# Optimization experiments

Measured on AMD Instinct MI355X. Metric: run time of the kernel, lower is better.

Reference implementation:

```python
import jax, jax.numpy as jnp
import numpy as np
from jax import lax

B = 4096
D = 128
N = 81
H = 4
HD = D // H


def _conv(x, w, b, pad):
    y = lax.conv_general_dilated(x, w, (1, 1), [(pad, pad), (pad, pad)],
                                 dimension_numbers=('NCHW', 'OIHW', 'NCHW'))
    return y + b[None, :, None, None]


def _attn_mask():
    # per-head additive structural mask: same-row, same-col, same-box, global
    idx = jnp.arange(N)
    rows, cols = idx // 9, idx % 9
    boxes = rows // 3 * 3 + cols // 3
    same = lambda v: (v[:, None] == v[None, :]).astype(jnp.float32)
    return jnp.stack([same(rows), same(cols), same(boxes),
                      jnp.ones((N, N), jnp.float32)], 0)  # [4, 81, 81]


def setup_inputs():
    key = jax.random.key(0)
    ks = jax.random.split(key, 12)
    digits = jax.random.randint(ks[0], (B, 9, 9), 0, 10)
    s = jax.nn.one_hot(digits, 10, axis=1, dtype=jnp.float32)  # [B,10,9,9]

    def w(k, shape, fan):
        return jax.random.normal(k, shape, jnp.float32) / np.sqrt(fan)

    return {
        's': s,
        'c1_w': w(ks[1], (64, 10, 1, 1), 10), 'c1_b': jnp.zeros((64,)),
        'c2_w': w(ks[2], (128, 64, 3, 3), 64 * 9), 'c2_b': jnp.zeros((128,)),
        'c3_w': w(ks[3], (128, 128, 3, 3), 128 * 9), 'c3_b': jnp.zeros((128,)),
        'emb': 0.02 * jax.random.normal(ks[4], (1, N, D), jnp.float32),
        'in_w': w(ks[5], (3 * D, D), D), 'in_b': jnp.zeros((3 * D,)),
        'out_w': w(ks[6], (D, D), D), 'out_b': jnp.zeros((D,)),
        'ln_g': jnp.ones((D,)), 'ln_b': jnp.zeros((D,)),
        'l1_w': w(ks[7], (D, D), D), 'l1_b': jnp.zeros((D,)),
        'l2_w': w(ks[8], (D, D), D), 'l2_b': jnp.zeros((D,)),
        'pos_w': w(ks[9], (1, D), D), 'pos_b': jnp.zeros((1,)),
        'num_w': w(ks[10], (10, D), D), 'num_b': jnp.zeros((10,)),
    }


def reference(s, c1_w, c1_b, c2_w, c2_b, c3_w, c3_b, emb, in_w, in_b,
              out_w, out_b, ln_g, ln_b, l1_w, l1_b, l2_w, l2_b,
              pos_w, pos_b, num_w, num_b):
    # conv stem (note: no activation after c1, matching the torch code)
    x = _conv(s, c1_w, c1_b, 0)
    x = jax.nn.silu(_conv(x, c2_w, c2_b, 1))
    x = jax.nn.silu(_conv(x, c3_w, c3_b, 1))
    x = x.reshape(B, D, N).transpose(0, 2, 1) + emb  # [B,81,128]

    # MHA with per-head additive structural mask, no residual
    qkv = x @ in_w.T + in_b
    q, k, v = jnp.split(qkv, 3, axis=-1)
    heads = lambda t: t.reshape(B, N, H, HD).transpose(0, 2, 1, 3)
    q, k, v = heads(q), heads(k), heads(v)
    scores = jnp.einsum('bhqd,bhkd->bhqk', q, k) / np.sqrt(HD) + _attn_mask()[None]
    a = jax.nn.softmax(scores, axis=-1)          # [B,4,81,81]
    asc = a.mean(axis=1)                          # averaged attn weights
    ctx = jnp.einsum('bhqk,bhkd->bhqd', a, v).transpose(0, 2, 1, 3).reshape(B, N, D)
    x = ctx @ out_w.T + out_b

    # LayerNorm
    mu = x.mean(-1, keepdims=True)
    var = ((x - mu) ** 2).mean(-1, keepdims=True)
    x = (x - mu) / jnp.sqrt(var + 1e-5) * ln_g + ln_b

    x = jax.nn.silu(x @ l1_w.T + l1_b)
    x = jax.nn.silu(x @ l2_w.T + l2_b)

    # position head with masked softmax over empty cells
    pos_logits = (x @ pos_w.T + pos_b)[..., 0]    # [B,81]
    given = (s.argmax(1) != 0).reshape(B, N)
    pos_logits = jnp.where(given, -1e9, pos_logits)
    k1, k2 = jax.random.split(jax.random.key(42))
    pos = jax.random.categorical(k1, pos_logits)  # [B] int

    # number head at sampled position, digit 0 masked out
    num_logits = x @ num_w.T + num_b              # [B,81,10]
    o = jnp.take_along_axis(num_logits, pos[:, None, None], axis=1)[:, 0, :]
    o = o.at[:, 0].set(-jnp.inf)
    num = jax.random.categorical(k2, o)
    return pos, num, asc
```

## Files before the change

### kernel.cpp

```cpp
#include <hip/hip_runtime.h>
#include <stdint.h>
#include <math.h>


#define NB 4096

typedef unsigned short u16;
typedef _Float16 f16x8 __attribute__((ext_vector_type(8)));
typedef float f32x4 __attribute__((ext_vector_type(4)));

__device__ __forceinline__ float silu_f(float v) {
  return v / (1.0f + expf(-v));
}

__device__ __forceinline__ void splitu(float v, u16& h, u16& l) {
  _Float16 hf = (_Float16)v;
  _Float16 lf = (_Float16)((v - (float)hf) * 2048.0f);
  union { _Float16 f; u16 u; } a, b;
  a.f = hf; b.f = lf;
  h = a.u; l = b.u;
}

__device__ __forceinline__ float joinu(u16 h, u16 l) {
  union { u16 u; _Float16 f; } a, b;
  a.u = h; b.u = l;
  return (float)a.f + (float)b.f * (1.f/2048.f);
}

__device__ __forceinline__ void tf_round(uint32_t& x0, uint32_t& x1, int r) {
  x0 += x1;
  x1 = (x1 << r) | (x1 >> (32 - r));
  x1 ^= x0;
}

__device__ __forceinline__ void threefry2x32(uint32_t k0, uint32_t k1,
                                             uint32_t x0, uint32_t x1,
                                             uint32_t& o0, uint32_t& o1) {
  uint32_t k2 = k0 ^ k1 ^ 0x1BD11BDAu;
  x0 += k0; x1 += k1;
  tf_round(x0,x1,13); tf_round(x0,x1,15); tf_round(x0,x1,26); tf_round(x0,x1,6);
  x0 += k1; x1 += k2 + 1u;
  tf_round(x0,x1,17); tf_round(x0,x1,29); tf_round(x0,x1,16); tf_round(x0,x1,24);
  x0 += k2; x1 += k0 + 2u;
  tf_round(x0,x1,13); tf_round(x0,x1,15); tf_round(x0,x1,26); tf_round(x0,x1,6);
  x0 += k0; x1 += k1 + 3u;
  tf_round(x0,x1,17); tf_round(x0,x1,29); tf_round(x0,x1,16); tf_round(x0,x1,24);
  x0 += k1; x1 += k2 + 4u;
  tf_round(x0,x1,13); tf_round(x0,x1,15); tf_round(x0,x1,26); tf_round(x0,x1,6);
  x0 += k2; x1 += k0 + 5u;
  o0 = x0; o1 = x1;
}

__device__ __forceinline__ void jax_split42(uint32_t& k1a, uint32_t& k1b,
                                            uint32_t& k2a, uint32_t& k2b) {
  threefry2x32(0u, 42u, 0u, 0u, k1a, k1b);
  threefry2x32(0u, 42u, 0u, 1u, k2a, k2b);
}

__device__ __forceinline__ uint32_t jax_randbits(uint32_t ka, uint32_t kb,
                                                 uint32_t i) {
  uint32_t o0, o1;
  threefry2x32(ka, kb, 0u, i, o0, o1);
  return o0 ^ o1;
}

__device__ __forceinline__ float jax_gumbel_bits(uint32_t bits) {
  float f = __uint_as_float((bits >> 9) | 0x3f800000u) - 1.0f;
  const float tiny = 1.17549435e-38f;
  float u = fmaxf(tiny, f + tiny);
  return -logf(-logf(u));
}

__global__ __launch_bounds__(256) void k_prep(
    const float* __restrict__ c1_w, const float* __restrict__ c1_b,
    const float* __restrict__ c2_w, const float* __restrict__ c3_w,
    const float* __restrict__ out_w, const float* __restrict__ l1_w,
    const float* __restrict__ l2_w,
    float* __restrict__ T2e, u16* __restrict__ WAh, u16* __restrict__ WAl,
    u16* __restrict__ WOh, u16* __restrict__ W1h, u16* __restrict__ W2h)
{
  int idx = blockIdx.x * 256 + threadIdx.x;
  if (idx < 9*11*128) {
    int oc = idx & 127;
    int t  = idx >> 7;
    int g  = t % 11;
    int d  = t / 11;
    float acc = 0.f;
    if (g < 10) {
      int di = d / 3, dj = d % 3;
      for (int ic = 0; ic < 64; ++ic) {
        float x1 = c1_w[ic*10 + g] + c1_b[ic];
        acc += c2_w[((oc*64 + ic)*3 + di)*3 + dj] * x1;
      }
    }
    T2e[idx] = acc;
  } else if (idx < 160128) {
    int j  = idx - 12672;
    int jj = j & 7;
    int t  = j >> 3;
    int ln = t & 63;
    int t2 = t >> 6;
    int ot = t2 & 7;
    int t3 = t2 >> 3;
    int kc = t3 & 3;
    int d  = t3 >> 2;
    int oc = ot*16 + (ln & 15);
    int ic = kc*32 + (ln >> 4)*8 + jj;
    float w = c3_w[(oc*128 + ic)*9 + d];
    u16 wh, wl;
    splitu(w, wh, wl);
    WAh[j] = wh; WAl[j] = wl;
  } else if (idx < 209280) {
    int j = idx - 160128;
    int mi = j >> 14;
    int jr = j & 16383;
    int jj = jr & 7;
    int t  = jr >> 3;
    int ln = t & 63;
    int t2 = t >> 6;
    int ot = t2 & 7;
    int kc = t2 >> 3;
    int oc = ot*16 + (ln & 15);
    int k  = kc*32 + (ln >> 4)*8 + jj;
    const float* W = (mi == 0) ? out_w : (mi == 1) ? l1_w : l2_w;
    u16* Dh = (mi == 0) ? WOh : (mi == 1) ? W1h : W2h;
    u16 wh, wl;
    splitu(W[oc*128 + k], wh, wl);
    Dh[jr] = wh; Dh[16384 + jr] = wl;
  }
}

__global__ __launch_bounds__(256, 2) void k_stem(
    const float* __restrict__ s, const float* __restrict__ T2e,
    const float* __restrict__ c2_b,
    const u16* __restrict__ WAh, const u16* __restrict__ WAl,
    const float* __restrict__ c3_b, const float* __restrict__ emb,
    u16* __restrict__ xh, u16* __restrict__ xl, int* __restrict__ digits)
{
  __shared__ __align__(16) u16 x2h[121*128];
  __shared__ __align__(16) u16 x2l[121*128];
  __shared__ int dg[121];
  const int b   = blockIdx.x;
  const int tid = threadIdx.x;

  for (int i = tid; i < 1936; i += 256) {
    ((uint4*)x2h)[i] = make_uint4(0u,0u,0u,0u);
    ((uint4*)x2l)[i] = make_uint4(0u,0u,0u,0u);
  }
  if (tid < 121) dg[tid] = 10;
  __syncthreads();

  if (tid < 81) {
    const float* sp = s + (size_t)b*810 + tid;
    float dv = 0.f;
    #pragma unroll
    for (int c = 1; c < 10; ++c) dv += (float)c * sp[c*81];
    int d = (int)(dv + 0.5f);
    dg[(tid/9 + 1)*11 + (tid%9 + 1)] = d;
    digits[b*81 + tid] = d;
  }
  __syncthreads();

  for (int i = tid; i < 1296; i += 256) {
    const int p  = i >> 4;
    const int k8 = i & 15;
    const int r0 = p / 9, c0 = p - r0*9;
    const float4 b0 = *(const float4*)(c2_b + k8*8);
    const float4 b1 = *(const float4*)(c2_b + k8*8 + 4);
    float a0=b0.x, a1=b0.y, a2=b0.z, a3=b0.w;
    float a4=b1.x, a5=b1.y, a6=b1.z, a7=b1.w;
    #pragma unroll
    for (int d = 0; d < 9; ++d) {
      const int g = dg[(r0 + d/3)*11 + (c0 + d%3)];
      const float* tp = T2e + (size_t)(d*11 + g)*128 + k8*8;
      const float4 t0 = *(const float4*)tp;
      const float4 t1 = *(const float4*)(tp + 4);
      a0 += t0.x; a1 += t0.y; a2 += t0.z; a3 += t0.w;
      a4 += t1.x; a5 += t1.y; a6 += t1.z; a7 += t1.w;
    }
    float v[8];
    v[0]=silu_f(a0); v[1]=silu_f(a1); v[2]=silu_f(a2); v[3]=silu_f(a3);
    v[4]=silu_f(a4); v[5]=silu_f(a5); v[6]=silu_f(a6); v[7]=silu_f(a7);
    f16x8 hv, lv;
    #pragma unroll
    for (int j = 0; j < 8; ++j) {
      _Float16 h = (_Float16)v[j];
      hv[j] = h;
      lv[j] = (_Float16)((v[j] - (float)h) * 2048.0f);
    }
    const int row = (r0 + 1)*11 + (c0 + 1);
    const uint32_t bo = (uint32_t)row*256u + ((uint32_t)(k8 ^ (row & 15)) << 4);
    *(f16x8*)((char*)x2h + bo) = hv;
    *(f16x8*)((char*)x2l + bo) = lv;
  }
  __syncthreads();

  const int ln  = tid & 63;
  const int wv  = tid >> 6;
  const int lg  = ln >> 4;
  const int lr  = ln & 15;
  const int otB = (wv & 1) * 4;
  const int ntB = (wv >> 1) * 3;

  f32x4 accH[4][3];
  f32x4 accC[4][3];
  #pragma unroll
  for (int ot = 0; ot < 4; ++ot)
    #pragma unroll
    for (int nt = 0; nt < 3; ++nt) {
      accH[ot][nt] = (f32x4){0.f,0.f,0.f,0.f};
      accC[ot][nt] = (f32x4){0.f,0.f,0.f,0.f};
    }

  int pbase[3];
  #pragma unroll
  for (int nt = 0; nt < 3; ++nt) {
    const int c = (ntB + nt)*16 + lr;
    pbase[nt] = (c < 81) ? (c/9)*11 + (c%9) : 0;
  }
  const char* x2hB = (const char*)x2h;
  const char* x2lB = (const char*)x2l;

  for (int d = 0; d < 9; ++d) {
    const int off = (d/3)*11 + (d - (d/3)*3);
    int rowv[3];
    #pragma unroll
    for (int nt = 0; nt < 3; ++nt) rowv[nt] = pbase[nt] + off;
    #pragma unroll
    for (int kc = 0; kc < 4; ++kc) {
      f16x8 Bh[3], Bl[3];
      #pragma unroll
      for (int nt = 0; nt < 3; ++nt) {
        const uint32_t o = (uint32_t)rowv[nt]*256u +
            ((uint32_t)((kc*4 + lg) ^ (rowv[nt] & 15)) << 4);
        Bh[nt] = *(const f16x8*)(x2hB + o);
        Bl[nt] = *(const f16x8*)(x2lB + o);
      }
      const int abase = (((d*4 + kc)*8 + otB)*64 + ln)*8;
      f16x8 Ah[4], Al[4];
      #pragma unroll
      for (int ot = 0; ot < 4; ++ot) {
        Ah[ot] = *(const f16x8*)(WAh + abase + ot*512);
        Al[ot] = *(const f16x8*)(WAl + abase + ot*512);
      }
      #pragma unroll
      for (int ot = 0; ot < 4; ++ot)
        #pragma unroll
        for (int nt = 0; nt < 3; ++nt) {
          accH[ot][nt] = __builtin_amdgcn_mfma_f32_16x16x32_f16(
              Ah[ot], Bh[nt], accH[ot][nt], 0, 0, 0);
          accC[ot][nt] = __builtin_amdgcn_mfma_f32_16x16x32_f16(
              Ah[ot], Bl[nt], accC[ot][nt], 0, 0, 0);
          accC[ot][nt] = __builtin_amdgcn_mfma_f32_16x16x32_f16(
              Al[ot], Bh[nt], accC[ot][nt], 0, 0, 0);
        }
    }
  }

  #pragma unroll
  for (int nt = 0; nt < 3; ++nt) {
    const int cell = (ntB + nt)*16 + lr;
    if (cell < 81) {
      const size_t xoff = ((size_t)b*81 + cell)*128;
      #pragma unroll
      for (int ot = 0; ot < 4; ++ot) {
        const int oc = (otB + ot)*16 + lg*4;
        const float4 b3 = *(const float4*)(c3_b + oc);
        const float4 e  = *(const float4*)(emb + cell*128 + oc);
        const f32x4 hh = accH[ot][nt];
        const f32x4 cc = accC[ot][nt];
        float o0 = silu_f(hh[0] + cc[0]*(1.f/2048.f) + b3.x) + e.x;
        float o1 = silu_f(hh[1] + cc[1]*(1.f/2048.f) + b3.y) + e.y;
        float o2 = silu_f(hh[2] + cc[2]*(1.f/2048.f) + b3.z) + e.z;
        float o3 = silu_f(hh[3] + cc[3]*(1.f/2048.f) + b3.w) + e.w;
        ushort4 hv, lv;
        splitu(o0, hv.x, lv.x); splitu(o1, hv.y, lv.y);
        splitu(o2, hv.z, lv.z); splitu(o3, hv.w, lv.w);
        *(ushort4*)(xh + xoff + oc) = hv;
        *(ushort4*)(xl + xoff + oc) = lv;
      }
    }
  }
}

#define ATTN_LDS_BYTES 141568

__global__ __launch_bounds__(512, 1) void k_attn(
    const u16* __restrict__ xhg, const u16* __restrict__ xlg,
    const float* __restrict__ in_w, const float* __restrict__ in_b,
    u16* __restrict__ ctxh, u16* __restrict__ ctxl, float* __restrict__ asc)
{
  extern __shared__ char smc[];
  char*  XH   = smc;
  char*  XL   = smc + 24576;
  char*  QK   = smc + 49152;
  char*  VTH  = smc + 73728;
  char*  VTL  = smc + 81920;
  float* SC   = (float*)(smc + 90112);
  char*  PH   = smc + 90112;
  char*  PL   = smc + 114688;
  float* RINV = (float*)(smc + 140800);
  uint32_t* RCB = (uint32_t*)(smc + 141184);

  const int b   = blockIdx.x;
  const int tid = threadIdx.x;
  const int ln  = tid & 63;
  const int wv  = tid >> 6;
  const int lg  = ln >> 4;
  const int lr  = ln & 15;

  if (tid < 96) {
    const int r = tid/9, c = tid - r*9;
    const int bx = (r/3)*3 + c/3;
    RCB[tid] = (uint32_t)r | ((uint32_t)c << 8) | ((uint32_t)bx << 16);
  }
  {
    const u16* gx = xhg + (size_t)b*81*128;
    const u16* gl = xlg + (size_t)b*81*128;
    for (int i = tid; i < 1296; i += 512) {
      const int n = i >> 4, k8 = i & 15;
      const uint4 hv = *(const uint4*)(gx + n*128 + k8*8);
      const uint4 lv = *(const uint4*)(gl + n*128 + k8*8);
      const uint32_t bo = (uint32_t)n*256u + ((uint32_t)(k8 ^ (n & 15)) << 4);
      *(uint4*)(XH + bo) = hv;
      *(uint4*)(XL + bo) = lv;
    }
    for (int i = tid; i < 480; i += 512) {
      char* base = (i < 240) ? XH : XL;
      const int j = (i < 240) ? i : (i - 240);
      *(uint4*)(base + 81*256 + j*16) = make_uint4(0u,0u,0u,0u);
    }
  }

  float ascR[16];
  #pragma unroll
  for (int i = 0; i < 16; ++i) ascR[i] = 0.f;

  __syncthreads();

  for (int h = 0; h < 4; ++h) {
    if (wv < 6) {
      const int part = wv >> 1;
      const int sub  = wv & 1;
      const int rowbase = part*128 + h*32 + sub*16;
      f32x4 accH[6], accC[6];
      #pragma unroll
      for (int nt = 0; nt < 6; ++nt) {
        accH[nt] = (f32x4){0.f,0.f,0.f,0.f};
        accC[nt] = (f32x4){0.f,0.f,0.f,0.f};
      }
      for (int kc = 0; kc < 4; ++kc) {
        const float* wp = in_w + (size_t)(rowbase + lr)*128 + kc*32 + lg*8;
        f16x8 Ah, Al;
        #pragma unroll
        for (int j = 0; j < 8; ++j) {
          const float w = wp[j];
          const _Float16 hf = (_Float16)w;
          Ah[j] = hf;
          Al[j] = (_Float16)((w - (float)hf) * 2048.0f);
        }
        #pragma unroll
        for (int nt = 0; nt < 6; ++nt) {
          const int row = nt*16 + lr;
          const uint32_t o = (uint32_t)row*256u +
              ((uint32_t)((kc*4 + lg) ^ (row & 15)) << 4);
          const f16x8 Bh = *(const f16x8*)(XH + o);
          const f16x8 Bl = *(const f16x8*)(XL + o);
          accH[nt] = __builtin_amdgcn_mfma_f32_16x16x32_f16(Ah, Bh, accH[nt], 0,0,0);
          accC[nt] = __builtin_amdgcn_mfma_f32_16x16x32_f16(Ah, Bl, accC[nt], 0,0,0);
          accC[nt] = __builtin_amdgcn_mfma_f32_16x16x32_f16(Al, Bh, accC[nt], 0,0,0);
        }
      }
      const float4 bia = *(const float4*)(in_b + rowbase + lg*4);
      #pragma unroll
      for (int nt = 0; nt < 6; ++nt) {
        const int cell = nt*16 + lr;
        float v0 = accH[nt][0] + accC[nt][0]*(1.f/2048.f) + bia.x;
        float v1 = accH[nt][1] + accC[nt][1]*(1.f/2048.f) + bia.y;
        float v2 = accH[nt][2] + accC[nt][2]*(1.f/2048.f) + bia.z;
        float v3 = accH[nt][3] + accC[nt][3]*(1.f/2048.f) + bia.w;
        if (part < 2) {
          ushort4 hw, lw;
          splitu(v0, hw.x, lw.x); splitu(v1, hw.y, lw.y);
          splitu(v2, hw.z, lw.z); splitu(v3, hw.w, lw.w);
          const int sflat = part*4 + sub*2 + (lg >> 1);
          const int byo   = (lg & 1)*8;
          const uint32_t adH = (uint32_t)cell*256u +
              ((uint32_t)(sflat ^ (cell & 15)) << 4) + byo;
          const uint32_t adL = (uint32_t)cell*256u +
              ((uint32_t)((8 + sflat) ^ (cell & 15)) << 4) + byo;
          *(ushort4*)(QK + adH) = hw;
          *(ushort4*)(QK + adL) = lw;
        } else {
          float vv[4] = {v0, v1, v2, v3};
          #pragma unroll
          for (int r = 0; r < 4; ++r) {
            const int hd = sub*16 + lg*4 + r;
            u16 hh, llv;
            splitu(vv[r], hh, llv);
            const uint32_t ad = (uint32_t)hd*256u +
                ((uint32_t)((cell >> 3) ^ (hd & 15)) << 4) + (cell & 7)*2;
            *(u16*)(VTH + ad) = hh;
            *(u16*)(VTL + ad) = llv;
          }
        }
      }
    }
    __syncthreads();

    {
      const uint32_t mb = (h==0) ? 0xFFu : (h==1) ? 0xFF00u
                        : (h==2) ? 0xFF0000u : 0u;
      const int t0 = (wv*36) >> 3, t1 = ((wv + 1)*36) >> 3;
      for (int t = t0; t < t1; ++t) {
        const int qt = t/6, nt = t - (t/6)*6;
        const int ra = qt*16 + lr;
        const f16x8 Qh = *(const f16x8*)(QK + (uint32_t)ra*256u +
            ((uint32_t)(lg ^ (ra & 15)) << 4));
        const f16x8 Ql = *(const f16x8*)(QK + (uint32_t)ra*256u +
            ((uint32_t)((8 + lg) ^ (ra & 15)) << 4));
        const int rb = nt*16 + lr;
        const f16x8 Kh = *(const f16x8*)(QK + (uint32_t)rb*256u +
            ((uint32_t)((4 + lg) ^ (rb & 15)) << 4));
        const f16x8 Kl = *(const f16x8*)(QK + (uint32_t)rb*256u +
            ((uint32_t)((12 + lg) ^ (rb & 15)) << 4));
        f32x4 aH = (f32x4){0.f,0.f,0.f,0.f};
        f32x4 aC = (f32x4){0.f,0.f,0.f,0.f};
        aH = __builtin_amdgcn_mfma_f32_16x16x32_f16(Qh, Kh, aH, 0,0,0);
        aC = __builtin_amdgcn_mfma_f32_16x16x32_f16(Qh, Kl, aC, 0,0,0);
        aC = __builtin_amdgcn_mfma_f32_16x16x32_f16(Ql, Kh, aC, 0,0,0);
        const int kcell = nt*16 + lr;
        const uint32_t kk = RCB[kcell];
        #pragma unroll
        for (int r = 0; r < 4; ++r) {
          const int q = qt*16 + lg*4 + r;
          const uint32_t qq = RCB[q];
          const float msk = (((qq ^ kk) & mb) == 0u) ? 1.f : 0.f;
          SC[q*132 + kcell] =
              (aH[r] + aC[r]*(1.f/2048.f)) * 0.17677669529663687f + msk;
        }
      }
    }
    __syncthreads();

    if (tid < 324) {
      const int row = tid >> 2, sub = tid & 3;
      float* sr = SC + row*132;
      const int kb = sub*24;
      const int ke = (sub == 3) ? 81 : kb + 24;
      float m = -1e30f;
      for (int k = kb; k < ke; ++k) m = fmaxf(m, sr[k]);
      m = fmaxf(m, __shfl_xor(m, 1));
      m = fmaxf(m, __shfl_xor(m, 2));
      float ss = 0.f;
      for (int k = kb; k < ke; ++k) {
        const float e = __expf(sr[k] - m);
        sr[k] = e;
        ss += e;
      }
      if (sub == 3) {
        #pragma unroll
        for (int k = 81; k < 96; ++k) sr[k] = 0.f;
      }
      ss += __shfl_xor(ss, 1);
      ss += __shfl_xor(ss, 2);
      if (sub == 0) RINV[row] = 1.0f / ss;
    }
    __syncthreads();

    float pa[2][8];
    #pragma unroll
    for (int i = 0; i < 2; ++i) {
      const int idx = tid + i*512;
      if (idx < 972) {
        const int q = idx / 12, k8 = idx - q*12;
        const float rv = RINV[q];
        const float* sp = SC + q*132 + k8*8;
        const float4 p0 = *(const float4*)sp;
        const float4 p1 = *(const float4*)(sp + 4);
        pa[i][0] = p0.x*rv; pa[i][1] = p0.y*rv;
        pa[i][2] = p0.z*rv; pa[i][3] = p0.w*rv;
        pa[i][4] = p1.x*rv; pa[i][5] = p1.y*rv;
        pa[i][6] = p1.z*rv; pa[i][7] = p1.w*rv;
        #pragma unroll
        for (int j = 0; j < 8; ++j) ascR[i*8 + j] += pa[i][j];
      }
    }
    __syncthreads();
    #pragma unroll
    for (int i = 0; i < 2; ++i) {
      const int idx = tid + i*512;
      if (idx < 972) {
        const int q = idx / 12, k8 = idx - q*12;
        union { u16 u[8]; uint4 v; } hw, lw;
        #pragma unroll
        for (int j = 0; j < 8; ++j) splitu(pa[i][j], hw.u[j], lw.u[j]);
        const uint32_t ad = (uint32_t)q*256u +
            ((uint32_t)(k8 ^ (q & 15)) << 4);
        *(uint4*)(PH + ad) = hw.v;
        *(uint4*)(PL + ad) = lw.v;
      }
    }
    __syncthreads();

    for (int t = wv; t < 12; t += 8) {
      const int ot = t/6, nt = t - (t/6)*6;
      f32x4 aH = (f32x4){0.f,0.f,0.f,0.f};
      f32x4 aC = (f32x4){0.f,0.f,0.f,0.f};
      #pragma unroll
      for (int kc = 0; kc < 3; ++kc) {
        const int ra = ot*16 + lr;
        const uint32_t oa = (uint32_t)ra*256u +
            ((uint32_t)((kc*4 + lg) ^ (ra & 15)) << 4);
        const f16x8 Vh = *(const f16x8*)(VTH + oa);
        const f16x8 Vl = *(const f16x8*)(VTL + oa);
        const int rb = nt*16 + lr;
        const uint32_t ob = (uint32_t)rb*256u +
            ((uint32_t)((kc*4 + lg) ^ (rb & 15)) << 4);
        const f16x8 Pf  = *(const f16x8*)(PH + ob);
        const f16x8 Pl2 = *(const f16x8*)(PL + ob);
        aH = __builtin_amdgcn_mfma_f32_16x16x32_f16(Vh, Pf,  aH, 0,0,0);
        aC = __builtin_amdgcn_mfma_f32_16x16x32_f16(Vh, Pl2, aC, 0,0,0);
        aC = __builtin_amdgcn_mfma_f32_16x16x32_f16(Vl, Pf,  aC, 0,0,0);
      }
      const int cell = nt*16 + lr;
      if (cell < 81) {
        const size_t co = ((size_t)b*81 + cell)*128 + h*32 + ot*16 + lg*4;
        ushort4 hw, lw;
        float r0 = aH[0] + aC[0]*(1.f/2048.f);
        float r1 = aH[1] + aC[1]*(1.f/2048.f);
        float r2 = aH[2] + aC[2]*(1.f/2048.f);
        float r3 = aH[3] + aC[3]*(1.f/2048.f);
        splitu(r0, hw.x, lw.x); splitu(r1, hw.y, lw.y);
        splitu(r2, hw.z, lw.z); splitu(r3, hw.w, lw.w);
        *(ushort4*)(ctxh + co) = hw;
        *(ushort4*)(ctxl + co) = lw;
      }
    }
    __syncthreads();
  }

  #pragma unroll
  for (int i = 0; i < 2; ++i) {
    const int idx = tid + i*512;
    if (idx < 972) {
      const int q = idx / 12, k8 = idx - q*12;
      #pragma unroll
      for (int j = 0; j < 8; ++j) {
        const int k = k8*8 + j;
        if (k < 81) asc[(size_t)b*6561 + q*81 + k] = 0.25f * ascR[i*8 + j];
      }
    }
  }
}

#define POST_LDS_BYTES 105664

__global__ __launch_bounds__(512, 1) void k_post(
    const u16* __restrict__ ctxh, const u16* __restrict__ ctxl,
    const u16* __restrict__ WOh,  const float* __restrict__ out_b,
    const float* __restrict__ ln_g, const float* __restrict__ ln_b,
    const u16* __restrict__ W1h,  const float* __restrict__ l1_b,
    const u16* __restrict__ W2h,  const float* __restrict__ l2_b,
    const float* __restrict__ pos_w, const float* __restrict__ pos_b,
    const float* __restrict__ num_w, const float* __restrict__ num_b,
    const int* __restrict__ digits,  float* __restrict__ dout)
{
  extern __shared__ char smc[];
  char*  YH   = smc;
  char*  YL   = smc + 24576;
  char*  ZH   = smc + 49152;
  char*  ZL   = smc + 73728;
  float* red1 = (float*)(smc + 98304);
  float* red2 = (float*)(smc + 101376);
  float* mu   = (float*)(smc + 104448);
  float* rstd = (float*)(smc + 104832);
  float* vals = (float*)(smc + 105216);
  int*   posi = (int*)(smc + 105600);

  const int b   = blockIdx.x;
  const int tid = threadIdx.x;
  const int ln  = tid & 63;
  const int wv  = tid >> 6;
  const int lg  = ln >> 4;
  const int lr  = ln & 15;
  const int ocb = wv*16 + lg*4;

  {
    const u16* gh = ctxh + (size_t)b*81*128;
    const u16* gl = ctxl + (size_t)b*81*128;
    for (int i = tid; i < 1296; i += 512) {
      const int n = i >> 4, k8 = i & 15;
      const uint4 hv = *(const uint4*)(gh + n*128 + k8*8);
      const uint4 lv = *(const uint4*)(gl + n*128 + k8*8);
      const uint32_t bo = (uint32_t)n*256u + ((uint32_t)(k8 ^ (n & 15)) << 4);
      *(uint4*)(YH + bo) = hv;
      *(uint4*)(YL + bo) = lv;
    }
    for (int i = tid; i < 480; i += 512) {
      char* base = (i < 240) ? YH : YL;
      const int j = (i < 240) ? i : (i - 240);
      *(uint4*)(base + 81*256 + j*16) = make_uint4(0u,0u,0u,0u);
    }
  }
  __syncthreads();

  f32x4 aH[6], aC[6];
  #define GEMM6(BH, BL, WT)                                               \
    {                                                                     \
      _Pragma("unroll")                                                   \
      for (int nt = 0; nt < 6; ++nt) {                                    \
        aH[nt] = (f32x4){0.f,0.f,0.f,0.f};                                \
        aC[nt] = (f32x4){0.f,0.f,0.f,0.f};                                \
      }                                                                   \
      for (int kc = 0; kc < 4; ++kc) {                                    \
        const int ab = ((kc*8 + wv)*64 + ln)*8;                           \
        const f16x8 Ah = *(const f16x8*)((WT) + ab);                      \
        const f16x8 Al = *(const f16x8*)((WT) + 16384 + ab);              \
        _Pragma("unroll")                                                 \
        for (int nt = 0; nt < 6; ++nt) {                                  \
          const int row = nt*16 + lr;                                     \
          const uint32_t o = (uint32_t)row*256u +                         \
              ((uint32_t)((kc*4 + lg) ^ (row & 15)) << 4);                \
          const f16x8 Bh = *(const f16x8*)((BH) + o);                     \
          const f16x8 Bl = *(const f16x8*)((BL) + o);                     \
          aH[nt] = __builtin_amdgcn_mfma_f32_16x16x32_f16(Ah, Bh, aH[nt], 0,0,0); \
          aC[nt] = __builtin_amdgcn_mfma_f32_16x16x32_f16(Ah, Bl, aC[nt], 0,0,0); \
          aC[nt] = __builtin_amdgcn_mfma_f32_16x16x32_f16(Al, Bh, aC[nt], 0,0,0); \
        }                                                                 \
      }                                                                   \
    }

  GEMM6(YH, YL, WOh);
  float y[6][4];
  {
    const float4 bv = *(const float4*)(out_b + ocb);
    #pragma unroll
    for (int nt = 0; nt < 6; ++nt) {
      y[nt][0] = aH[nt][0] + aC[nt][0]*(1.f/2048.f) + bv.x;
      y[nt][1] = aH[nt][1] + aC[nt][1]*(1.f/2048.f) + bv.y;
      y[nt][2] = aH[nt][2] + aC[nt][2]*(1.f/2048.f) + bv.z;
      y[nt][3] = aH[nt][3] + aC[nt][3]*(1.f/2048.f) + bv.w;
    }
  }

  #pragma unroll
  for (int nt = 0; nt < 6; ++nt) {
    float s1 = y[nt][0] + y[nt][1] + y[nt][2] + y[nt][3];
    s1 += __shfl_xor(s1, 16);
    s1 += __shfl_xor(s1, 32);
    if (ln < 16) red1[(nt*16 + lr)*8 + wv] = s1;
  }
  __syncthreads();
  if (tid < 96) {
    float s = 0.f;
    #pragma unroll
    for (int w = 0; w < 8; ++w) s += red1[tid*8 + w];
    mu[tid] = s * (1.0f/128.0f);
  }
  __syncthreads();
  #pragma unroll
  for (int nt = 0; nt < 6; ++nt) {
    const float m = mu[nt*16 + lr];
    float d0 = y[nt][0]-m, d1 = y[nt][1]-m, d2 = y[nt][2]-m, d3 = y[nt][3]-m;
    float s2 = d0*d0 + d1*d1 + d2*d2 + d3*d3;
    s2 += __shfl_xor(s2, 16);
    s2 += __shfl_xor(s2, 32);
    if (ln < 16) red2[(nt*16 + lr)*8 + wv] = s2;
  }
  __syncthreads();
  if (tid < 96) {
    float s = 0.f;
    #pragma unroll
    for (int w = 0; w < 8; ++w) s += red2[tid*8 + w];
    rstd[tid] = 1.0f / sqrtf(s * (1.0f/128.0f) + 1e-5f);
  }
  __syncthreads();
  {
    const float4 g  = *(const float4*)(ln_g + ocb);
    const float4 bb = *(const float4*)(ln_b + ocb);
    #pragma unroll
    for (int nt = 0; nt < 6; ++nt) {
      const int cell = nt*16 + lr;
      const float m = mu[cell], rs = rstd[cell];
      float z0 = (y[nt][0]-m)*rs*g.x + bb.x;
      float z1 = (y[nt][1]-m)*rs*g.y + bb.y;
      float z2 = (y[nt][2]-m)*rs*g.z + bb.z;
      float z3 = (y[nt][3]-m)*rs*g.w + bb.w;
      ushort4 hw, lw;
      splitu(z0, hw.x, lw.x); splitu(z1, hw.y, lw.y);
      splitu(z2, hw.z, lw.z); splitu(z3, hw.w, lw.w);
      const uint32_t ad = (uint32_t)cell*256u +
          ((uint32_t)((wv*2 + (lg >> 1)) ^ (cell & 15)) << 4) + (lg & 1)*8;
      *(ushort4*)(ZH + ad) = hw;
      *(ushort4*)(ZL + ad) = lw;
    }
  }
  __syncthreads();

  GEMM6(ZH, ZL, W1h);
  {
    const float4 bv = *(const float4*)(l1_b + ocb);
    #pragma unroll
    for (int nt = 0; nt < 6; ++nt) {
      const int cell = nt*16 + lr;
      float z0 = silu_f(aH[nt][0] + aC[nt][0]*(1.f/2048.f) + bv.x);
      float z1 = silu_f(aH[nt][1] + aC[nt][1]*(1.f/2048.f) + bv.y);
      float z2 = silu_f(aH[nt][2] + aC[nt][2]*(1.f/2048.f) + bv.z);
      float z3 = silu_f(aH[nt][3] + aC[nt][3]*(1.f/2048.f) + bv.w);
      ushort4 hw, lw;
      splitu(z0, hw.x, lw.x); splitu(z1, hw.y, lw.y);
      splitu(z2, hw.z, lw.z); splitu(z3, hw.w, lw.w);
      const uint32_t ad = (uint32_t)cell*256u +
          ((uint32_t)((wv*2 + (lg >> 1)) ^ (cell & 15)) << 4) + (lg & 1)*8;
      *(ushort4*)(YH + ad) = hw;
      *(ushort4*)(YL + ad) = lw;
    }
  }
  __syncthreads();

  GEMM6(YH, YL, W2h);
  {
    const float4 bv = *(const float4*)(l2_b + ocb);
    const float4 pw = *(const float4*)(pos_w + ocb);
    #pragma unroll
    for (int nt = 0; nt < 6; ++nt) {
      const int cell = nt*16 + lr;
      float z0 = silu_f(aH[nt][0] + aC[nt][0]*(1.f/2048.f) + bv.x);
      float z1 = silu_f(aH[nt][1] + aC[nt][1]*(1.f/2048.f) + bv.y);
      float z2 = silu_f(aH[nt][2] + aC[nt][2]*(1.f/2048.f) + bv.z);
      float z3 = silu_f(aH[nt][3] + aC[nt][3]*(1.f/2048.f) + bv.w);
      ushort4 hw, lw;
      splitu(z0, hw.x, lw.x); splitu(z1, hw.y, lw.y);
      splitu(z2, hw.z, lw.z); splitu(z3, hw.w, lw.w);
      const uint32_t ad = (uint32_t)cell*256u +
          ((uint32_t)((wv*2 + (lg >> 1)) ^ (cell & 15)) << 4) + (lg & 1)*8;
      *(ushort4*)(ZH + ad) = hw;
      *(ushort4*)(ZL + ad) = lw;
      float ps = z0*pw.x + z1*pw.y + z2*pw.z + z3*pw.w;
      ps += __shfl_xor(ps, 16);
      ps += __shfl_xor(ps, 32);
      if (ln < 16) red1[cell*8 + wv] = ps;
    }
  }
  __syncthreads();

  uint32_t k1a, k1b, k2a, k2b;
  jax_split42(k1a, k1b, k2a, k2b);

  if (tid < 81) {
    float acc = pos_b[0];
    #pragma unroll
    for (int w = 0; w < 8; ++w) acc += red1[tid*8 + w];
    if (digits[b*81 + tid] != 0) acc = -1e9f;
    uint32_t bits = jax_randbits(k1a, k1b, (uint32_t)(b*81 + tid));
    vals[tid] = acc + jax_gumbel_bits(bits);
  }
  __syncthreads();
  if (tid == 0) {
    float best = vals[0]; int bi = 0;
    for (int n = 1; n < 81; ++n)
      if (vals[n] > best) { best = vals[n]; bi = n; }
    *posi = bi;
    dout[b] = (float)bi;
  }
  __syncthreads();
  const int pos = *posi;

  if (tid < 80) {
    const int d = tid >> 3, j = tid & 7;
    float ssum = 0.f;
    #pragma unroll
    for (int c = 0; c < 16; ++c) {
      const int k = j*16 + c;
      const uint32_t ad = (uint32_t)pos*256u +
          ((uint32_t)((k >> 3) ^ (pos & 15)) << 4) + (k & 7)*2;
      const float yv = joinu(*(const u16*)(ZH + ad), *(const u16*)(ZL + ad));
      ssum += yv * num_w[d*128 + k];
    }
    red2[tid] = ssum;
  }
  __syncthreads();
  if (tid < 10) {
    float acc = num_b[tid];
    #pragma unroll
    for (int j = 0; j < 8; ++j) acc += red2[tid*8 + j];
    if (tid == 0) acc = -INFINITY;
    uint32_t bits = jax_randbits(k2a, k2b, (uint32_t)(b*10 + tid));
    vals[tid] = acc + jax_gumbel_bits(bits);
  }
  __syncthreads();
  if (tid == 0) {
    float best = vals[0]; int bi = 0;
    for (int d = 1; d < 10; ++d)
      if (vals[d] > best) { best = vals[d]; bi = d; }
    dout[NB + b] = (float)bi;
  }
}

extern "C" void kernel_launch(void* const* d_in, const int* in_sizes, int n_in,
                              void* d_out, int out_size, void* d_ws, size_t ws_size,
                              hipStream_t stream) {
  const float* s     = (const float*)d_in[0];
  const float* c1_w  = (const float*)d_in[1];
  const float* c1_b  = (const float*)d_in[2];
  const float* c2_w  = (const float*)d_in[3];
  const float* c2_b  = (const float*)d_in[4];
  const float* c3_w  = (const float*)d_in[5];
  const float* c3_b  = (const float*)d_in[6];
  const float* emb   = (const float*)d_in[7];
  const float* in_w  = (const float*)d_in[8];
  const float* in_b  = (const float*)d_in[9];
  const float* out_w = (const float*)d_in[10];
  const float* out_b = (const float*)d_in[11];
  const float* ln_g  = (const float*)d_in[12];
  const float* ln_b  = (const float*)d_in[13];
  const float* l1_w  = (const float*)d_in[14];
  const float* l1_b  = (const float*)d_in[15];
  const float* l2_w  = (const float*)d_in[16];
  const float* l2_b  = (const float*)d_in[17];
  const float* pos_w = (const float*)d_in[18];
  const float* pos_b = (const float*)d_in[19];
  const float* num_w = (const float*)d_in[20];
  const float* num_b = (const float*)d_in[21];

  float* ws     = (float*)d_ws;
  float* T2e    = ws;
  u16*   WAh    = (u16*)(ws + 12672);
  u16*   WAl    = (u16*)(ws + 86400);
  u16*   WOh    = (u16*)(ws + 160128);
  u16*   W1h    = (u16*)(ws + 176512);
  u16*   W2h    = (u16*)(ws + 192896);
  int*   digits = (int*)(ws + 209280);
  u16*   xh     = (u16*)(ws + 541056);
  u16*   xl     = (u16*)(ws + 21774720);
  u16*   ctxh   = (u16*)(ws + 43008384);
  u16*   ctxl   = (u16*)(ws + 43008384 + 21233664);

  float* dout = (float*)d_out;
  float* asc  = dout + 2*NB;

  hipFuncSetAttribute((const void*)k_attn,
                      hipFuncAttributeMaxDynamicSharedMemorySize,
                      ATTN_LDS_BYTES);
  hipFuncSetAttribute((const void*)k_post,
                      hipFuncAttributeMaxDynamicSharedMemorySize,
                      POST_LDS_BYTES);

  k_prep<<<dim3(818), dim3(256), 0, stream>>>(
      c1_w, c1_b, c2_w, c3_w, out_w, l1_w, l2_w,
      T2e, WAh, WAl, WOh, W1h, W2h);
  k_stem<<<dim3(NB), dim3(256), 0, stream>>>(
      s, T2e, c2_b, WAh, WAl, c3_b, emb, xh, xl, digits);
  k_attn<<<dim3(NB), dim3(512), ATTN_LDS_BYTES, stream>>>(
      xh, xl, in_w, in_b, ctxh, ctxl, asc);
  k_post<<<dim3(NB), dim3(512), POST_LDS_BYTES, stream>>>(
      ctxh, ctxl, WOh, out_b, ln_g, ln_b, W1h, l1_b, W2h, l2_b,
      pos_w, pos_b, num_w, num_b, digits, dout);
}
```

Baseline: 1.440 ms.

## Presplit QKV weights in prep, spread QKV tiles over all waves, keep softmax in registers

The in_proj weights are now split into fp16 hi/lo once in k_prep, stored in MFMA fragment order, and loaded directly as vectors instead of being converted from fp32 per block and head. The QKV projection is split into 36 tile units spread across all 8 waves instead of 6, and each wave reuses B fragments cached in registers. Softmax keeps the row values in registers and fuses normalization, asc accumulation and the P store into one pass. This removes the RINV buffer and one barrier per head. Register pressure rises (e[24], ascR[24], B fragment arrays), which could limit scheduling.

```diff
diff --git a/kernel.cpp b/kernel.cpp
--- a/kernel.cpp
+++ b/kernel.cpp
@@ -74,9 +74,11 @@
 __global__ __launch_bounds__(256) void k_prep(
     const float* __restrict__ c1_w, const float* __restrict__ c1_b,
     const float* __restrict__ c2_w, const float* __restrict__ c3_w,
+    const float* __restrict__ in_w,
     const float* __restrict__ out_w, const float* __restrict__ l1_w,
     const float* __restrict__ l2_w,
     float* __restrict__ T2e, u16* __restrict__ WAh, u16* __restrict__ WAl,
+    u16* __restrict__ WIh, u16* __restrict__ WIl,
     u16* __restrict__ WOh, u16* __restrict__ W1h, u16* __restrict__ W2h)
 {
   int idx = blockIdx.x * 256 + threadIdx.x;
@@ -127,6 +129,22 @@
     u16 wh, wl;
     splitu(W[oc*128 + k], wh, wl);
     Dh[jr] = wh; Dh[16384 + jr] = wl;
+  } else if (idx < 258432) {
+    int j  = idx - 209280;
+    int jj = j & 7;
+    int t  = j >> 3;
+    int ln = t & 63;
+    int t2 = t >> 6;
+    int kc = t2 & 3;
+    int t3 = t2 >> 2;
+    int h  = t3 / 6;
+    int pu = t3 - h*6;
+    int part = pu >> 1, sub = pu & 1;
+    int row = part*128 + h*32 + sub*16 + (ln & 15);
+    int k   = kc*32 + (ln >> 4)*8 + jj;
+    u16 wh, wl;
+    splitu(in_w[row*128 + k], wh, wl);
+    WIh[j] = wh; WIl[j] = wl;
   }
 }
 
@@ -287,7 +305,8 @@
 
 __global__ __launch_bounds__(512, 1) void k_attn(
     const u16* __restrict__ xhg, const u16* __restrict__ xlg,
-    const float* __restrict__ in_w, const float* __restrict__ in_b,
+    const u16* __restrict__ WIh, const u16* __restrict__ WIl,
+    const float* __restrict__ in_b,
     u16* __restrict__ ctxh, u16* __restrict__ ctxl, float* __restrict__ asc)
 {
   extern __shared__ char smc[];
@@ -299,7 +318,6 @@
   float* SC   = (float*)(smc + 90112);
   char*  PH   = smc + 90112;
   char*  PL   = smc + 114688;
-  float* RINV = (float*)(smc + 140800);
   uint32_t* RCB = (uint32_t*)(smc + 141184);
 
   const int b   = blockIdx.x;
@@ -332,53 +350,53 @@
     }
   }
 
-  float ascR[16];
+  const int srow = tid >> 2;
+  const int ssub = tid & 3;
+  const int skn  = (ssub == 3) ? 9 : 24;
+  float ascR[24];
   #pragma unroll
-  for (int i = 0; i < 16; ++i) ascR[i] = 0.f;
+  for (int i = 0; i < 24; ++i) ascR[i] = 0.f;
 
   __syncthreads();
 
   for (int h = 0; h < 4; ++h) {
-    if (wv < 6) {
-      const int part = wv >> 1;
-      const int sub  = wv & 1;
-      const int rowbase = part*128 + h*32 + sub*16;
-      f32x4 accH[6], accC[6];
-      #pragma unroll
-      for (int nt = 0; nt < 6; ++nt) {
-        accH[nt] = (f32x4){0.f,0.f,0.f,0.f};
-        accC[nt] = (f32x4){0.f,0.f,0.f,0.f};
-      }
-      for (int kc = 0; kc < 4; ++kc) {
-        const float* wp = in_w + (size_t)(rowbase + lr)*128 + kc*32 + lg*8;
-        f16x8 Ah, Al;
+    {
+      const int t0 = (wv*36) >> 3, t1 = ((wv + 1)*36) >> 3;
+      int curNt = -1;
+      f16x8 Bh[4], Bl[4];
+      for (int u = t0; u < t1; ++u) {
+        const int nt = u/6, pu = u - (u/6)*6;
+        if (nt != curNt) {
+          curNt = nt;
+          const int row = nt*16 + lr;
+          #pragma unroll
+          for (int kc = 0; kc < 4; ++kc) {
+            const uint32_t o = (uint32_t)row*256u +
+                ((uint32_t)((kc*4 + lg) ^ (row & 15)) << 4);
+            Bh[kc] = *(const f16x8*)(XH + o);
+            Bl[kc] = *(const f16x8*)(XL + o);
+          }
+        }
+        const int part = pu >> 1, sub = pu & 1;
+        const int rowbase = part*128 + h*32 + sub*16;
+        const u16* wph = WIh + (size_t)((h*6 + pu)*4)*512 + ln*8;
+        const u16* wpl = WIl + (size_t)((h*6 + pu)*4)*512 + ln*8;
+        f32x4 aH = (f32x4){0.f,0.f,0.f,0.f};
+        f32x4 aC = (f32x4){0.f,0.f,0.f,0.f};
         #pragma unroll
-        for (int j = 0; j < 8; ++j) {
-          const float w = wp[j];
-          const _Float16 hf = (_Float16)w;
-          Ah[j] = hf;
-          Al[j] = (_Float16)((w - (float)hf) * 2048.0f);
+        for (int kc = 0; kc < 4; ++kc) {
+          const f16x8 Ah = *(const f16x8*)(wph + kc*512);
+          const f16x8 Al = *(const f16x8*)(wpl + kc*512);
+          aH = __builtin_amdgcn_mfma_f32_16x16x32_f16(Ah, Bh[kc], aH, 0,0,0);
+          aC = __builtin_amdgcn_mfma_f32_16x16x32_f16(Ah, Bl[kc], aC, 0,0,0);
+          aC = __builtin_amdgcn_mfma_f32_16x16x32_f16(Al, Bh[kc], aC, 0,0,0);
         }
-        #pragma unroll
-        for (int nt = 0; nt < 6; ++nt) {
-          const int row = nt*16 + lr;
-          const uint32_t o = (uint32_t)row*256u +
-              ((uint32_t)((kc*4 + lg) ^ (row & 15)) << 4);
-          const f16x8 Bh = *(const f16x8*)(XH + o);
-          const f16x8 Bl = *(const f16x8*)(XL + o);
-          accH[nt] = __builtin_amdgcn_mfma_f32_16x16x32_f16(Ah, Bh, accH[nt], 0,0,0);
-          accC[nt] = __builtin_amdgcn_mfma_f32_16x16x32_f16(Ah, Bl, accC[nt], 0,0,0);
-          accC[nt] = __builtin_amdgcn_mfma_f32_16x16x32_f16(Al, Bh, accC[nt], 0,0,0);
-        }
-      }
-      const float4 bia = *(const float4*)(in_b + rowbase + lg*4);
-      #pragma unroll
-      for (int nt = 0; nt < 6; ++nt) {
+        const float4 bia = *(const float4*)(in_b + rowbase + lg*4);
+        const float v0 = aH[0] + aC[0]*(1.f/2048.f) + bia.x;
+        const float v1 = aH[1] + aC[1]*(1.f/2048.f) + bia.y;
+        const float v2 = aH[2] + aC[2]*(1.f/2048.f) + bia.z;
+        const float v3 = aH[3] + aC[3]*(1.f/2048.f) + bia.w;
         const int cell = nt*16 + lr;
-        float v0 = accH[nt][0] + accC[nt][0]*(1.f/2048.f) + bia.x;
-        float v1 = accH[nt][1] + accC[nt][1]*(1.f/2048.f) + bia.y;
-        float v2 = accH[nt][2] + accC[nt][2]*(1.f/2048.f) + bia.z;
-        float v3 = accH[nt][3] + accC[nt][3]*(1.f/2048.f) + bia.w;
         if (part < 2) {
           ushort4 hw, lw;
           splitu(v0, hw.x, lw.x); splitu(v1, hw.y, lw.y);
@@ -392,7 +410,7 @@
           *(ushort4*)(QK + adH) = hw;
           *(ushort4*)(QK + adL) = lw;
         } else {
-          float vv[4] = {v0, v1, v2, v3};
+          const float vv[4] = {v0, v1, v2, v3};
           #pragma unroll
           for (int r = 0; r < 4; ++r) {
             const int hd = sub*16 + lg*4 + r;
@@ -443,60 +461,46 @@
     }
     __syncthreads();
 
+    float e[24];
+    float rinv = 0.f;
     if (tid < 324) {
-      const int row = tid >> 2, sub = tid & 3;
-      float* sr = SC + row*132;
-      const int kb = sub*24;
-      const int ke = (sub == 3) ? 81 : kb + 24;
+      const float* sr = SC + srow*132 + ssub*24;
+      #pragma unroll
+      for (int q4 = 0; q4 < 6; ++q4) {
+        const float4 v = *(const float4*)(sr + q4*4);
+        e[q4*4+0] = v.x; e[q4*4+1] = v.y; e[q4*4+2] = v.z; e[q4*4+3] = v.w;
+      }
       float m = -1e30f;
-      for (int k = kb; k < ke; ++k) m = fmaxf(m, sr[k]);
+      #pragma unroll
+      for (int c = 0; c < 24; ++c)
+        if (c < skn) m = fmaxf(m, e[c]);
       m = fmaxf(m, __shfl_xor(m, 1));
       m = fmaxf(m, __shfl_xor(m, 2));
       float ss = 0.f;
-      for (int k = kb; k < ke; ++k) {
-        const float e = __expf(sr[k] - m);
-        sr[k] = e;
-        ss += e;
-      }
-      if (sub == 3) {
-        #pragma unroll
-        for (int k = 81; k < 96; ++k) sr[k] = 0.f;
+      #pragma unroll
+      for (int c = 0; c < 24; ++c) {
+        const float ex = (c < skn) ? __expf(e[c] - m) : 0.f;
+        e[c] = ex;
+        ss += ex;
       }
       ss += __shfl_xor(ss, 1);
       ss += __shfl_xor(ss, 2);
-      if (sub == 0) RINV[row] = 1.0f / ss;
+      rinv = 1.0f / ss;
     }
     __syncthreads();
-
-    float pa[2][8];
-    #pragma unroll
-    for (int i = 0; i < 2; ++i) {
-      const int idx = tid + i*512;
-      if (idx < 972) {
-        const int q = idx / 12, k8 = idx - q*12;
-        const float rv = RINV[q];
-        const float* sp = SC + q*132 + k8*8;
-        const float4 p0 = *(const float4*)sp;
-        const float4 p1 = *(const float4*)(sp + 4);
-        pa[i][0] = p0.x*rv; pa[i][1] = p0.y*rv;
-        pa[i][2] = p0.z*rv; pa[i][3] = p0.w*rv;
-        pa[i][4] = p1.x*rv; pa[i][5] = p1.y*rv;
-        pa[i][6] = p1.z*rv; pa[i][7] = p1.w*rv;
-        #pragma unroll
-        for (int j = 0; j < 8; ++j) ascR[i*8 + j] += pa[i][j];
-      }
-    }
-    __syncthreads();
-    #pragma unroll
-    for (int i = 0; i < 2; ++i) {
-      const int idx = tid + i*512;
-      if (idx < 972) {
-        const int q = idx / 12, k8 = idx - q*12;
+    if (tid < 324) {
+      #pragma unroll
+      for (int cc = 0; cc < 3; ++cc) {
+        const int c8 = ssub*3 + cc;
         union { u16 u[8]; uint4 v; } hw, lw;
         #pragma unroll
-        for (int j = 0; j < 8; ++j) splitu(pa[i][j], hw.u[j], lw.u[j]);
-        const uint32_t ad = (uint32_t)q*256u +
-            ((uint32_t)(k8 ^ (q & 15)) << 4);
+        for (int j = 0; j < 8; ++j) {
+          const float p = e[cc*8 + j] * rinv;
+          ascR[cc*8 + j] += p;
+          splitu(p, hw.u[j], lw.u[j]);
+        }
+        const uint32_t ad = (uint32_t)srow*256u +
+            ((uint32_t)(c8 ^ (srow & 15)) << 4);
         *(uint4*)(PH + ad) = hw.v;
         *(uint4*)(PL + ad) = lw.v;
       }
@@ -540,17 +544,11 @@
     __syncthreads();
   }
 
-  #pragma unroll
-  for (int i = 0; i < 2; ++i) {
-    const int idx = tid + i*512;
-    if (idx < 972) {
-      const int q = idx / 12, k8 = idx - q*12;
-      #pragma unroll
-      for (int j = 0; j < 8; ++j) {
-        const int k = k8*8 + j;
-        if (k < 81) asc[(size_t)b*6561 + q*81 + k] = 0.25f * ascR[i*8 + j];
-      }
-    }
+  if (tid < 324) {
+    float* ap = asc + (size_t)b*6561 + srow*81 + ssub*24;
+    #pragma unroll
+    for (int c = 0; c < 24; ++c)
+      if (c < skn) ap[c] = 0.25f * ascR[c];
   }
 }
 
@@ -831,7 +829,9 @@
   u16*   WOh    = (u16*)(ws + 160128);
   u16*   W1h    = (u16*)(ws + 176512);
   u16*   W2h    = (u16*)(ws + 192896);
-  int*   digits = (int*)(ws + 209280);
+  u16*   WIh    = (u16*)(ws + 209280);
+  u16*   WIl    = (u16*)(ws + 233856);
+  int*   digits = (int*)(ws + 258432);
   u16*   xh     = (u16*)(ws + 541056);
   u16*   xl     = (u16*)(ws + 21774720);
   u16*   ctxh   = (u16*)(ws + 43008384);
@@ -847,13 +847,13 @@
                       hipFuncAttributeMaxDynamicSharedMemorySize,
                       POST_LDS_BYTES);
 
-  k_prep<<<dim3(818), dim3(256), 0, stream>>>(
-      c1_w, c1_b, c2_w, c3_w, out_w, l1_w, l2_w,
-      T2e, WAh, WAl, WOh, W1h, W2h);
+  k_prep<<<dim3(1010), dim3(256), 0, stream>>>(
+      c1_w, c1_b, c2_w, c3_w, in_w, out_w, l1_w, l2_w,
+      T2e, WAh, WAl, WIh, WIl, WOh, W1h, W2h);
   k_stem<<<dim3(NB), dim3(256), 0, stream>>>(
       s, T2e, c2_b, WAh, WAl, c3_b, emb, xh, xl, digits);
   k_attn<<<dim3(NB), dim3(512), ATTN_LDS_BYTES, stream>>>(
-      xh, xl, in_w, in_b, ctxh, ctxl, asc);
+      xh, xl, WIh, WIl, in_b, ctxh, ctxl, asc);
   k_post<<<dim3(NB), dim3(512), POST_LDS_BYTES, stream>>>(
       ctxh, ctxl, WOh, out_b, ln_g, ln_b, W1h, l1_b, W2h, l2_b,
       pos_w, pos_b, num_w, num_b, digits, dout);
```

After: 1.421 ms. About the same (-1.3%).
